# Optimization experiments

Hardware: AMD Instinct MI355X
Metric: run time of the kernel (lower is better)

## Reference

```python
import jax, jax.numpy as jnp
import numpy as np

LN_EPS = 1e-5

def _layer_norm(x, w, b):
    mu = jnp.mean(x, axis=-1, keepdims=True)
    var = jnp.mean(jnp.square(x - mu), axis=-1, keepdims=True)
    return (x - mu) * jax.lax.rsqrt(var + LN_EPS) * w + b

def setup_inputs() -> dict:
    key = jax.random.key(0)
    ks = jax.random.split(key, 8)
    B, NODES, D = 32, 202, 64
    return {
        "embeddings": jax.random.normal(ks[0], (B, NODES, D), dtype=jnp.float32),
        "ln_w": jnp.ones((D,), jnp.float32),
        "ln_b": jnp.zeros((D,), jnp.float32),
        "W1_w": jax.random.normal(ks[1], (D, D), jnp.float32) * 0.05,
        "W1_b": jax.random.normal(ks[2], (D,), jnp.float32) * 0.05,
        "W2_w": jax.random.normal(ks[3], (D, D), jnp.float32) * 0.05,
        "W2_b": jax.random.normal(ks[4], (D,), jnp.float32) * 0.05,
        "a1_w": jax.random.normal(ks[5], (3 * D,), jnp.float32) * 0.05,
        "a1_b": jax.random.normal(ks[6], (1,), jnp.float32) * 0.05,
        "a2_w": jax.random.normal(ks[7], (3 * D,), jnp.float32) * 0.05,
        "a2_b": jax.random.normal(jax.random.fold_in(key, 99), (1,), jnp.float32) * 0.05,
    }

def reference(embeddings, ln_w, ln_b, W1_w, W1_b, W2_w, W2_b, a1_w, a1_b, a2_w, a2_b):
    # embeddings: [B, 2+N, D]; dropout p=0 (eval) -> identity
    emb = _layer_norm(embeddings, ln_w, ln_b)
    uid0 = emb[:, 0, :]          # [B, D]
    iid0 = emb[:, 1, :]          # [B, D]
    iatt = emb[:, 2:, :]         # [B, N, D]
    ua = uid0[:, None, :] * iatt  # [B, N, D]
    # value[b,i,j,:] = LN(ua[b,i] * ua[b,j])  -- the big [B,N,N,D] tensor
    value = _layer_norm(ua[:, :, None, :] * ua[:, None, :, :], ln_w, ln_b)

    def head(Ww, Wb, aw, ab):
        # Linear W applied to expanded query/key/iid collapses to per-row projections;
        # a([wq; wk; wiid]) decomposes additively across the three concat blocks.
        wua = ua @ Ww.T + Wb                  # [B, N, D]  (shared by query rows and key cols)
        wiid = iid0 @ Ww.T + Wb               # [B, D]
        aq, ak, ai = jnp.split(aw, 3)
        sq = wua @ aq                         # [B, N]  query contribution (index i)
        sk = wua @ ak                         # [B, N]  key contribution (index j)
        si = wiid @ ai                        # [B]
        scores = sq[:, :, None] + sk[:, None, :] + si[:, None, None] + ab[0]  # [B,N,N]
        scores = jax.nn.leaky_relu(scores)    # negative_slope=0.01 (torch default)
        alphas = jax.nn.softmax(scores, axis=-1)
        # original sums over dim=-2 (index i), softmax was over j -- kept faithfully
        return jnp.einsum('bij,bijd->bjd', alphas, value)  # [B, N, D]

    att1 = head(W1_w, W1_b, a1_w, a1_b)
    att2 = head(W2_w, W2_b, a2_w, a2_b)
    att_value = (att1 + att2) * 0.5           # [B, N, D]
    ui = (uid0 * iid0)[:, None, :]            # [B, 1, D]
    em_out = jnp.concatenate([ui, att_value], axis=1)  # [B, N+1, D]
    return jax.nn.leaky_relu(em_out)
```

## Files before the change

kernel.cpp:

```cpp
#include <hip/hip_runtime.h>
#include <hip/hip_bf16.h>

#define LN_EPS 1e-5f
#define BB 32
#define NI 200
#define DD 64

typedef __attribute__((ext_vector_type(8))) short bf16x8;
typedef __attribute__((ext_vector_type(4))) short bf16x4;
typedef __attribute__((ext_vector_type(4))) float f32x4;

__device__ __forceinline__ float leaky(float x) { return fmaxf(x, 0.01f * x); }
__device__ __forceinline__ short f2bf(float x) {
  __hip_bfloat16 h = __float2bfloat16(x);
  return *reinterpret_cast<short*>(&h);
}
__device__ __forceinline__ float bf2fs(short s) {
  unsigned u = ((unsigned)(unsigned short)s) << 16;
  return __uint_as_float(u);
}

__device__ __forceinline__ void reduce2(float& a, float& b) {
#pragma unroll
  for (int m = 1; m < 64; m <<= 1) { a += __shfl_xor(a, m, 64); b += __shfl_xor(b, m, 64); }
}
__device__ __forceinline__ void reduce3(float& a, float& b, float& c) {
#pragma unroll
  for (int m = 1; m < 64; m <<= 1) {
    a += __shfl_xor(a, m, 64); b += __shfl_xor(b, m, 64); c += __shfl_xor(c, m, 64);
  }
}
__device__ __forceinline__ void rmax2(float& a, float& b) {
#pragma unroll
  for (int m = 1; m < 64; m <<= 1) {
    a = fmaxf(a, __shfl_xor(a, m, 64));
    b = fmaxf(b, __shfl_xor(b, m, 64));
  }
}

#define WB_STRIDE 88576
#define WB_UA2    26624
#define WB_UAT    53248
#define WB_ST     81920
#define WB_KV     86912
#define WX_RAWD   2834432
#define WX_TD     2940928
#define WX_CR     2941184

__global__ void __launch_bounds__(256)
gat_k1(const float* __restrict__ emb,
       const float* __restrict__ lw,
       const float* __restrict__ lb,
       const float* __restrict__ W1,
       const float* __restrict__ W1b,
       const float* __restrict__ W2,
       const float* __restrict__ W2b,
       const float* __restrict__ a1,
       const float* __restrict__ a2,
       float* __restrict__ ws,
       float* __restrict__ out) {
  __shared__ float sE[18 * 65];
  __shared__ float sV[4 * 64];
  __shared__ float sVi[2 * 64];
  __shared__ float sLN[18 * 2];

  int b = blockIdx.y, it = blockIdx.x, tid = threadIdx.x;
  int wv = tid >> 6, lane = tid & 63;

  char* wsb = (char*)ws + (size_t)b * WB_STRIDE;
  short* wUA  = (short*)wsb;
  short* wUA2 = (short*)(wsb + WB_UA2);
  short* wUAT = (short*)(wsb + WB_UAT);
  float* wRAW = (float*)((char*)ws + WX_RAWD) + (size_t)b * 832;
  float* wTD  = (float*)((char*)ws + WX_TD) + b * 2;
  float* wCR  = (float*)((char*)ws + WX_CR) + b * 6;

  for (int idx = tid; idx < 288; idx += 256) {
    int r = idx >> 4, qd = (idx & 15) << 2;
    int g = (r < 2) ? r : 2 + it * 16 + (r - 2);
    f32x4 v = {0, 0, 0, 0};
    if (g <= 201) v = *(const f32x4*)(emb + ((size_t)b * 202 + g) * 64 + qd);
    float* dst = sE + r * 65 + qd;
    dst[0] = v.x; dst[1] = v.y; dst[2] = v.z; dst[3] = v.w;
  }
  if (wv == 0) {
    float p0 = 0, p1 = 0;
#pragma unroll 8
    for (int d = 0; d < 64; d++) {
      float x = W1[d * 64 + lane];
      p0 = fmaf(x, a1[d], p0); p1 = fmaf(x, a1[64 + d], p1);
    }
    sV[0 * 64 + lane] = p0; sV[1 * 64 + lane] = p1;
  } else if (wv == 1) {
    float p0 = 0, p1 = 0;
#pragma unroll 8
    for (int d = 0; d < 64; d++) {
      float x = W2[d * 64 + lane];
      p0 = fmaf(x, a2[d], p0); p1 = fmaf(x, a2[64 + d], p1);
    }
    sV[2 * 64 + lane] = p0; sV[3 * 64 + lane] = p1;
  } else if (wv == 2 && it == 0) {
    float p = 0;
#pragma unroll 8
    for (int d = 0; d < 64; d++) p = fmaf(W1[d * 64 + lane], a1[128 + d], p);
    sVi[lane] = p;
    float c0 = W1b[lane] * a1[lane];
    float c1 = W1b[lane] * a1[64 + lane];
    float c2 = W1b[lane] * a1[128 + lane];
    reduce3(c0, c1, c2);
    if (lane == 0) { wCR[0] = c0; wCR[1] = c1; wCR[2] = c2; }
  } else if (wv == 3 && it == 0) {
    float p = 0;
#pragma unroll 8
    for (int d = 0; d < 64; d++) p = fmaf(W2[d * 64 + lane], a2[128 + d], p);
    sVi[64 + lane] = p;
    float c3 = W2b[lane] * a2[lane];
    float c4 = W2b[lane] * a2[64 + lane];
    float c5 = W2b[lane] * a2[128 + lane];
    reduce3(c3, c4, c5);
    if (lane == 0) { wCR[3] = c3; wCR[4] = c4; wCR[5] = c5; }
  }
  __syncthreads();

  {
    int o = tid & 7, rr = tid >> 3;
    float s = 0.f, s2 = 0.f;
    if (rr < 18) {
      const float* xr = sE + rr * 65 + o * 8;
#pragma unroll
      for (int k = 0; k < 8; k++) { float x = xr[k]; s += x; s2 = fmaf(x, x, s2); }
    }
#pragma unroll
    for (int m = 1; m < 8; m <<= 1) {
      s += __shfl_xor(s, m, 64); s2 += __shfl_xor(s2, m, 64);
    }
    if (rr < 18 && o == 0) {
      float mu = s * (1.f / 64);
      float var = fmaxf(s2 * (1.f / 64) - mu * mu, 0.f);
      sLN[rr * 2] = mu;
      sLN[rr * 2 + 1] = rsqrtf(var + LN_EPS);
    }
  }
  __syncthreads();

  {
    int d = tid & 63;
    float w = lw[d], bi = lb[d];
    for (int idx = tid; idx < 18 * 64; idx += 256) {
      int r = idx >> 6;
      float mu = sLN[r * 2], rinv = sLN[r * 2 + 1];
      float x = sE[r * 65 + d];
      sE[r * 65 + d] = (x - mu) * rinv * w + bi;
    }
  }
  __syncthreads();

  if (it == 0 && wv == 2) {
    float u0 = sE[lane], iid = sE[65 + lane];
    out[(size_t)(b * 201) * 64 + lane] = leaky(u0 * iid);
    float q0 = iid * sVi[lane], q1 = iid * sVi[64 + lane];
    reduce2(q0, q1);
    if (lane == 0) { wTD[0] = q0; wTD[1] = q1; }
  }
  if (tid < 128) {
    int rem = tid, kh = rem >> 6, ln = rem & 63;
    int lnode = ln & 15, g = it * 16 + lnode;
    int dbase = kh * 32 + (ln >> 4) * 8, lr = 2 + lnode;
    bf16x8 pk, pk2;
    if (g < NI) {
      const float* yr = sE + lr * 65 + dbase;
#pragma unroll
      for (int k = 0; k < 8; k++) {
        float v = sE[dbase + k] * yr[k];
        short h = f2bf(v);
        pk[k] = h;
        float f = bf2fs(h);
        pk2[k] = f2bf(f * f);
      }
    } else {
#pragma unroll
      for (int k = 0; k < 8; k++) { pk[k] = 0; pk2[k] = 0; }
    }
    *(bf16x8*)(wUA + (it * 128 + rem) * 8) = pk;
    *(bf16x8*)(wUA2 + (it * 128 + rem) * 8) = pk2;
  } else {
    int tid2 = tid - 128, d = tid2 & 63;
    int ir = (it & 1) * 2 + (tid2 >> 6), p = it >> 1;
    int i0 = p * 32 + ir * 8, ln0 = i0 - it * 16;
    float ud = sE[d];
    bf16x8 pk;
#pragma unroll
    for (int uu = 0; uu < 8; uu++) {
      int node = i0 + uu;
      pk[uu] = (node < NI) ? f2bf(ud * sE[(2 + ln0 + uu) * 65 + d]) : (short)0;
    }
    int off = ((p * 4 + (d >> 4)) * 64 + ((d & 15) + 16 * ir)) * 8;
    *(bf16x8*)(wUAT + off) = pk;
    if (it == 12) {
      bf16x8 z;
#pragma unroll
      for (int uu = 0; uu < 8; uu++) z[uu] = 0;
      int off2 = ((p * 4 + (d >> 4)) * 64 + ((d & 15) + 16 * (ir + 2))) * 8;
      *(bf16x8*)(wUAT + off2) = z;
    }
  }
  if (tid < 128) {
    int o = tid & 7, rr = tid >> 3;
    int i = it * 16 + rr;
    if (i < NI) {
      float uv0[8], uv1[8], uv2[8], uv3[8];
#pragma unroll
      for (int k = 0; k < 8; k++) {
        float u0k = sE[o * 8 + k];
        uv0[k] = u0k * sV[0 * 64 + o * 8 + k];
        uv1[k] = u0k * sV[1 * 64 + o * 8 + k];
        uv2[k] = u0k * sV[2 * 64 + o * 8 + k];
        uv3[k] = u0k * sV[3 * 64 + o * 8 + k];
      }
      const float* yr = sE + (2 + rr) * 65 + o * 8;
      float p0 = 0, p1 = 0, p2 = 0, p3 = 0;
#pragma unroll
      for (int k = 0; k < 8; k++) {
        float y = yr[k];
        p0 = fmaf(y, uv0[k], p0); p1 = fmaf(y, uv1[k], p1);
        p2 = fmaf(y, uv2[k], p2); p3 = fmaf(y, uv3[k], p3);
      }
#pragma unroll
      for (int m = 1; m < 8; m <<= 1) {
        p0 += __shfl_xor(p0, m, 64); p1 += __shfl_xor(p1, m, 64);
        p2 += __shfl_xor(p2, m, 64); p3 += __shfl_xor(p3, m, 64);
      }
      if (o == 0) {
        wRAW[i * 4 + 0] = p0; wRAW[i * 4 + 1] = p1;
        wRAW[i * 4 + 2] = p2; wRAW[i * 4 + 3] = p3;
      }
    }
  }
}

__global__ void __launch_bounds__(512)
gat_k2(float* __restrict__ ws,
       const float* __restrict__ a1b,
       const float* __restrict__ a2b) {
  __shared__ float skv[2 * 208];
  __shared__ float wmx[16];
  int b = blockIdx.y, bx = blockIdx.x, tid = threadIdx.x;
  int wv = tid >> 6, lane = tid & 63;

  char* wsb = (char*)ws + (size_t)b * WB_STRIDE;
  float* wST = (float*)(wsb + WB_ST);
  float* wKV = (float*)(wsb + WB_KV);
  const float* wRAW = (const float*)((char*)ws + WX_RAWD) + (size_t)b * 832;
  const float* wTD  = (const float*)((char*)ws + WX_TD) + b * 2;
  const float* wCR  = (const float*)((char*)ws + WX_CR) + b * 6;

  float c0 = wCR[0], c1 = wCR[1], c2 = wCR[2];
  float c3 = wCR[3], c4 = wCR[4], c5 = wCR[5];
  float t1 = (wTD[0] + c2) + a1b[0];
  float t2 = (wTD[1] + c5) + a2b[0];

  if (tid < 208) {
    float s1 = 0.f, s2 = 0.f;
    if (tid < NI) {
      s1 = wRAW[tid * 4 + 1] + c1;
      s2 = wRAW[tid * 4 + 3] + c4;
    }
    skv[tid] = s1; skv[208 + tid] = s2;
    if (bx == 0) { wKV[tid] = s1; wKV[208 + tid] = s2; }
  }
  __syncthreads();

  {
    float m1 = (tid < NI) ? skv[tid] : -3e38f;
    float m2 = (tid < NI) ? skv[208 + tid] : -3e38f;
    rmax2(m1, m2);
    if (lane == 0) { wmx[wv * 2] = m1; wmx[wv * 2 + 1] = m2; }
  }
  __syncthreads();

  {
    int o = tid & 3, item = tid >> 2;
    int rl = item >> 1, sh = item & 1;
    if (rl < 52) {
      int r = bx * 52 + rl;
      if (r < 208) {
        float* st = wST + r * 6 + sh * 3;
        if (r < NI) {
          float mx = -3e38f;
#pragma unroll
          for (int k = 0; k < 8; k++) mx = fmaxf(mx, wmx[k * 2 + sh]);
          float base = (wRAW[r * 4 + (sh ? 2 : 0)] + (sh ? c3 : c0)) + (sh ? t2 : t1);
          float rm = leaky(base + mx);
          const float* skh = skv + sh * 208;
          float den = 0.f;
          int j0 = o * 50;
#pragma unroll 5
          for (int j = j0; j < j0 + 50; j++) {
            float s = base + skh[j];
            den += __expf(fmaxf(s, 0.01f * s) - rm);
          }
          den += __shfl_xor(den, 1, 64);
          den += __shfl_xor(den, 2, 64);
          if (o == 0) { st[0] = base; st[1] = rm; st[2] = 1.0f / den; }
        } else if (o == 0) {
          st[0] = 0.f; st[1] = 0.f; st[2] = 0.f;
        }
      }
    }
  }
}

#define L_G1    7168
#define L_STAGE 14336
#define L_UA    14336
#define L_UA2   40960
#define L_UAT   67584
#define L_ST    96256
#define L_KV    101248
#define L_PART  102912
#define L_TOTAL 103936

__global__ void __launch_bounds__(512, 1)
gat_k3(const float* __restrict__ ws,
       const float* __restrict__ lw,
       const float* __restrict__ lb,
       float* __restrict__ out) {
  __shared__ __align__(16) char smem[L_TOTAL];
  short* sUA  = (short*)(smem + L_UA);
  short* sUA2 = (short*)(smem + L_UA2);
  short* sUAT = (short*)(smem + L_UAT);
  float* sST  = (float*)(smem + L_ST);
  float* sKV  = (float*)(smem + L_KV);
  float* sPart = (float*)(smem + L_PART);

  int b = blockIdx.y, bx = blockIdx.x, tid = threadIdx.x;
  int wv = tid >> 6, lane = tid & 63, q = lane >> 4, col = lane & 15;

  {
    const f32x4* src = (const f32x4*)((const char*)ws + (size_t)b * WB_STRIDE);
    f32x4* dst = (f32x4*)(smem + L_STAGE);
    for (int idx = tid; idx < WB_STRIDE / 16; idx += 512) dst[idx] = src[idx];
  }
  short* sG0 = (short*)smem;
  short* sG1 = (short*)(smem + L_G1);
  if (tid < 128) ((int*)sG0)[1664 + tid] = 0;
  else if (tid < 256) ((int*)sG1)[1664 + (tid - 128)] = 0;
  __syncthreads();

  int half = wv >> 2, wq = wv & 3;
  int jt = bx * 2 + half;
  bool act = (jt < 13);
  short* sGh = half ? sG1 : sG0;
  float* sPh = sPart + half * 128;

  if (act) {
    bf16x8 bf0 = *(bf16x8*)(sUA + ((jt * 2 + 0) * 64 + lane) * 8);
    bf16x8 bf1 = *(bf16x8*)(sUA + ((jt * 2 + 1) * 64 + lane) * 8);
    bf16x8 b2f0 = *(bf16x8*)(sUA2 + ((jt * 2 + 0) * 64 + lane) * 8);
    bf16x8 b2f1 = *(bf16x8*)(sUA2 + ((jt * 2 + 1) * 64 + lane) * 8);
    int jglob = jt * 16 + col;
    float skj1 = sKV[jglob], skj2 = sKV[208 + jglob];
    float mpart = 0.f, spart = 0.f;
    for (int it = wq; it < 13; it += 4) {
      bf16x8 af0 = *(bf16x8*)(sUA + ((it * 2 + 0) * 64 + lane) * 8);
      bf16x8 af1 = *(bf16x8*)(sUA + ((it * 2 + 1) * 64 + lane) * 8);
      bf16x8 a2f0 = *(bf16x8*)(sUA2 + ((it * 2 + 0) * 64 + lane) * 8);
      bf16x8 a2f1 = *(bf16x8*)(sUA2 + ((it * 2 + 1) * 64 + lane) * 8);
      f32x4 s = {0, 0, 0, 0}, t = {0, 0, 0, 0};
      s = __builtin_amdgcn_mfma_f32_16x16x32_bf16(af0, bf0, s, 0, 0, 0);
      s = __builtin_amdgcn_mfma_f32_16x16x32_bf16(af1, bf1, s, 0, 0, 0);
      t = __builtin_amdgcn_mfma_f32_16x16x32_bf16(a2f0, b2f0, t, 0, 0, 0);
      t = __builtin_amdgcn_mfma_f32_16x16x32_bf16(a2f1, b2f1, t, 0, 0, 0);
      bf16x4 gp;
#pragma unroll
      for (int r = 0; r < 4; r++) {
        int i = it * 16 + q * 4 + r;
        const float* st = sST + i * 6;
        float mu = s[r] * (1.f / 64);
        float var = fmaxf(t[r] * (1.f / 64) - mu * mu, 0.f);
        float inv = rsqrtf(var + LN_EPS);
        float sc1 = st[0] + skj1;
        float e1 = __expf(fmaxf(sc1, 0.01f * sc1) - st[1]) * st[2];
        float sc2 = st[3] + skj2;
        float e2 = __expf(fmaxf(sc2, 0.01f * sc2) - st[4]) * st[5];
        float c = 0.5f * (e1 + e2);
        float g = c * inv;
        mpart = fmaf(g, mu, mpart);
        spart += c;
        gp[r] = f2bf(g);
      }
      int kl = (it & 1) * 16 + q * 4;
      int off = ((it >> 1) * 64 + (col + 16 * (kl >> 3))) * 8 + (kl & 7);
      *(bf16x4*)(sGh + off) = gp;
    }
    mpart += __shfl_xor(mpart, 16, 64); mpart += __shfl_xor(mpart, 32, 64);
    spart += __shfl_xor(spart, 16, 64); spart += __shfl_xor(spart, 32, 64);
    if (lane < 16) {
      sPh[(wq * 2 + 0) * 16 + lane] = mpart;
      sPh[(wq * 2 + 1) * 16 + lane] = spart;
    }
  }
  __syncthreads();

  if (act) {
    f32x4 acc = {0, 0, 0, 0};
#pragma unroll
    for (int kt = 0; kt < 7; kt++) {
      bf16x8 ga = *(bf16x8*)(sGh + (kt * 64 + lane) * 8);
      bf16x8 ub = *(bf16x8*)(sUAT + ((kt * 4 + wq) * 64 + lane) * 8);
      acc = __builtin_amdgcn_mfma_f32_16x16x32_bf16(ga, ub, acc, 0, 0, 0);
    }
    int d = wq * 16 + col;
    float w = lw[d], bia = lb[d];
#pragma unroll
    for (int r = 0; r < 4; r++) {
      int jl = q * 4 + r, jg = jt * 16 + jl;
      if (jg < NI) {
        float m = sPh[0 * 16 + jl] + sPh[2 * 16 + jl] +
                  sPh[4 * 16 + jl] + sPh[6 * 16 + jl];
        float S = sPh[1 * 16 + jl] + sPh[3 * 16 + jl] +
                  sPh[5 * 16 + jl] + sPh[7 * 16 + jl];
        int cn = jt * 128 + (d >> 5) * 64 + ((d >> 3) & 3) * 16 + (jg & 15);
        float uajd = bf2fs(sUA[cn * 8 + (d & 7)]);
        float att = w * (uajd * acc[r] - m) + bia * S;
        out[(size_t)(b * 201 + 1 + jg) * 64 + d] = leaky(att);
      }
    }
  }
}

extern "C" void kernel_launch(void* const* d_in, const int* in_sizes, int n_in,
                              void* d_out, int out_size, void* d_ws, size_t ws_size,
                              hipStream_t stream) {
  const float* emb = (const float*)d_in[0];
  const float* lw  = (const float*)d_in[1];
  const float* lb  = (const float*)d_in[2];
  const float* W1  = (const float*)d_in[3];
  const float* W1b = (const float*)d_in[4];
  const float* W2  = (const float*)d_in[5];
  const float* W2b = (const float*)d_in[6];
  const float* a1  = (const float*)d_in[7];
  const float* a1b = (const float*)d_in[8];
  const float* a2  = (const float*)d_in[9];
  const float* a2b = (const float*)d_in[10];
  float* ws = (float*)d_ws;
  float* out = (float*)d_out;

  gat_k1<<<dim3(13, BB), dim3(256), 0, stream>>>(emb, lw, lb, W1, W1b, W2, W2b,
                                                 a1, a2, ws, out);
  gat_k2<<<dim3(4, BB), dim3(512), 0, stream>>>(ws, a1b, a2b);
  gat_k3<<<dim3(7, BB), dim3(512), 0, stream>>>(ws, lw, lb, out);
}
```

Measured before the change: 93.90 us.

## Fuse three kernels into one cooperative kernel with grid-wide syncs

Merges the three separate kernels into a single cooperative launch on a 7x32 grid of 512-thread blocks. Each block runs two former stage-1 tiles, one per half-block. Grid-wide syncs replace the kernel boundaries between the projection, softmax-statistics and attention stages. The softmax-denominator stage now spreads 30 rows per block across 7 blocks instead of 52 rows across 4. This removes two kernel launch gaps, at the cost of grid barrier overhead and a co-residency requirement of 224 blocks with about 104KB of LDS each.

```diff
diff --git a/kernel.cpp b/kernel.cpp
--- a/kernel.cpp
+++ b/kernel.cpp
@@ -1,5 +1,8 @@
 #include <hip/hip_runtime.h>
 #include <hip/hip_bf16.h>
+#include <hip/hip_cooperative_groups.h>
+
+namespace cg = cooperative_groups;
 
 #define LN_EPS 1e-5f
 #define BB 32
@@ -42,46 +45,77 @@
 #define WB_UA2    26624
 #define WB_UAT    53248
 #define WB_ST     81920
-#define WB_KV     86912
+#define WB_STAGE  86912
 #define WX_RAWD   2834432
 #define WX_TD     2940928
 #define WX_CR     2941184
 
-__global__ void __launch_bounds__(256)
-gat_k1(const float* __restrict__ emb,
-       const float* __restrict__ lw,
-       const float* __restrict__ lb,
-       const float* __restrict__ W1,
-       const float* __restrict__ W1b,
-       const float* __restrict__ W2,
-       const float* __restrict__ W2b,
-       const float* __restrict__ a1,
-       const float* __restrict__ a2,
-       float* __restrict__ ws,
-       float* __restrict__ out) {
-  __shared__ float sE[18 * 65];
-  __shared__ float sV[4 * 64];
-  __shared__ float sVi[2 * 64];
-  __shared__ float sLN[18 * 2];
-
-  int b = blockIdx.y, it = blockIdx.x, tid = threadIdx.x;
-  int wv = tid >> 6, lane = tid & 63;
+#define L_G1    7168
+#define L_SE0   0
+#define L_SE1   4680
+#define L_SV    9360
+#define L_SVI   10384
+#define L_SLN   10896
+#define L_STAGE 14336
+#define L_UA    14336
+#define L_UA2   40960
+#define L_UAT   67584
+#define L_ST    96256
+#define L_KV    101248
+#define L_PART  102912
+#define L_TOTAL 103936
+
+__global__ void __launch_bounds__(512, 1)
+gat_coop(const float* __restrict__ emb,
+         const float* __restrict__ lw,
+         const float* __restrict__ lb,
+         const float* __restrict__ W1,
+         const float* __restrict__ W1b,
+         const float* __restrict__ W2,
+         const float* __restrict__ W2b,
+         const float* __restrict__ a1,
+         const float* __restrict__ a1b,
+         const float* __restrict__ a2,
+         const float* __restrict__ a2b,
+         float* __restrict__ ws,
+         float* __restrict__ out) {
+  __shared__ __align__(16) char smem[L_TOTAL];
+  float* sV   = (float*)(smem + L_SV);
+  float* sVi  = (float*)(smem + L_SVI);
+  short* sUA  = (short*)(smem + L_UA);
+  short* sUA2 = (short*)(smem + L_UA2);
+  short* sUAT = (short*)(smem + L_UAT);
+  float* sST  = (float*)(smem + L_ST);
+  float* sKV  = (float*)(smem + L_KV);
+  float* sPart = (float*)(smem + L_PART);
+
+  int b = blockIdx.y, bx = blockIdx.x, tid = threadIdx.x;
+  int wv = tid >> 6, lane = tid & 63, q = lane >> 4, col = lane & 15;
+  int th = tid >> 8, t2 = tid & 255;
 
   char* wsb = (char*)ws + (size_t)b * WB_STRIDE;
   short* wUA  = (short*)wsb;
   short* wUA2 = (short*)(wsb + WB_UA2);
   short* wUAT = (short*)(wsb + WB_UAT);
+  float* wST  = (float*)(wsb + WB_ST);
   float* wRAW = (float*)((char*)ws + WX_RAWD) + (size_t)b * 832;
   float* wTD  = (float*)((char*)ws + WX_TD) + b * 2;
   float* wCR  = (float*)((char*)ws + WX_CR) + b * 6;
 
-  for (int idx = tid; idx < 288; idx += 256) {
-    int r = idx >> 4, qd = (idx & 15) << 2;
-    int g = (r < 2) ? r : 2 + it * 16 + (r - 2);
-    f32x4 v = {0, 0, 0, 0};
-    if (g <= 201) v = *(const f32x4*)(emb + ((size_t)b * 202 + g) * 64 + qd);
-    float* dst = sE + r * 65 + qd;
-    dst[0] = v.x; dst[1] = v.y; dst[2] = v.z; dst[3] = v.w;
+  int it = bx * 2 + th;
+  bool act1 = (it < 13);
+  float* sE = (float*)(smem + (th ? L_SE1 : L_SE0));
+  float* sLN = (float*)(smem + L_SLN) + th * 36;
+
+  if (act1) {
+    for (int idx = t2; idx < 288; idx += 256) {
+      int r = idx >> 4, qd = (idx & 15) << 2;
+      int g = (r < 2) ? r : 2 + it * 16 + (r - 2);
+      f32x4 v = {0, 0, 0, 0};
+      if (g <= 201) v = *(const f32x4*)(emb + ((size_t)b * 202 + g) * 64 + qd);
+      float* dst = sE + r * 65 + qd;
+      dst[0] = v.x; dst[1] = v.y; dst[2] = v.z; dst[3] = v.w;
+    }
   }
   if (wv == 0) {
     float p0 = 0, p1 = 0;
@@ -99,7 +133,7 @@
       p0 = fmaf(x, a2[d], p0); p1 = fmaf(x, a2[64 + d], p1);
     }
     sV[2 * 64 + lane] = p0; sV[3 * 64 + lane] = p1;
-  } else if (wv == 2 && it == 0) {
+  } else if (wv == 2 && bx == 0) {
     float p = 0;
 #pragma unroll 8
     for (int d = 0; d < 64; d++) p = fmaf(W1[d * 64 + lane], a1[128 + d], p);
@@ -109,7 +143,7 @@
     float c2 = W1b[lane] * a1[128 + lane];
     reduce3(c0, c1, c2);
     if (lane == 0) { wCR[0] = c0; wCR[1] = c1; wCR[2] = c2; }
-  } else if (wv == 3 && it == 0) {
+  } else if (wv == 3 && bx == 0) {
     float p = 0;
 #pragma unroll 8
     for (int d = 0; d < 64; d++) p = fmaf(W2[d * 64 + lane], a2[128 + d], p);
@@ -123,9 +157,9 @@
   __syncthreads();
 
   {
-    int o = tid & 7, rr = tid >> 3;
+    int o = t2 & 7, rr = t2 >> 3;
     float s = 0.f, s2 = 0.f;
-    if (rr < 18) {
+    if (act1 && rr < 18) {
       const float* xr = sE + rr * 65 + o * 8;
 #pragma unroll
       for (int k = 0; k < 8; k++) { float x = xr[k]; s += x; s2 = fmaf(x, x, s2); }
@@ -134,7 +168,7 @@
     for (int m = 1; m < 8; m <<= 1) {
       s += __shfl_xor(s, m, 64); s2 += __shfl_xor(s2, m, 64);
     }
-    if (rr < 18 && o == 0) {
+    if (act1 && rr < 18 && o == 0) {
       float mu = s * (1.f / 64);
       float var = fmaxf(s2 * (1.f / 64) - mu * mu, 0.f);
       sLN[rr * 2] = mu;
@@ -143,10 +177,10 @@
   }
   __syncthreads();
 
-  {
-    int d = tid & 63;
+  if (act1) {
+    int d = t2 & 63;
     float w = lw[d], bi = lb[d];
-    for (int idx = tid; idx < 18 * 64; idx += 256) {
+    for (int idx = t2; idx < 18 * 64; idx += 256) {
       int r = idx >> 6;
       float mu = sLN[r * 2], rinv = sLN[r * 2 + 1];
       float x = sE[r * 65 + d];
@@ -155,191 +189,156 @@
   }
   __syncthreads();
 
-  if (it == 0 && wv == 2) {
-    float u0 = sE[lane], iid = sE[65 + lane];
+  if (bx == 0 && wv == 2) {
+    const float* sE0 = (const float*)(smem + L_SE0);
+    float u0 = sE0[lane], iid = sE0[65 + lane];
     out[(size_t)(b * 201) * 64 + lane] = leaky(u0 * iid);
     float q0 = iid * sVi[lane], q1 = iid * sVi[64 + lane];
     reduce2(q0, q1);
     if (lane == 0) { wTD[0] = q0; wTD[1] = q1; }
   }
-  if (tid < 128) {
-    int rem = tid, kh = rem >> 6, ln = rem & 63;
-    int lnode = ln & 15, g = it * 16 + lnode;
-    int dbase = kh * 32 + (ln >> 4) * 8, lr = 2 + lnode;
-    bf16x8 pk, pk2;
-    if (g < NI) {
-      const float* yr = sE + lr * 65 + dbase;
-#pragma unroll
-      for (int k = 0; k < 8; k++) {
-        float v = sE[dbase + k] * yr[k];
-        short h = f2bf(v);
-        pk[k] = h;
-        float f = bf2fs(h);
-        pk2[k] = f2bf(f * f);
-      }
+  if (act1) {
+    if (t2 < 128) {
+      int rem = t2, kh = rem >> 6, ln = rem & 63;
+      int lnode = ln & 15, g = it * 16 + lnode;
+      int dbase = kh * 32 + (ln >> 4) * 8, lr = 2 + lnode;
+      bf16x8 pk, pk2;
+      if (g < NI) {
+        const float* yr = sE + lr * 65 + dbase;
+#pragma unroll
+        for (int k = 0; k < 8; k++) {
+          float v = sE[dbase + k] * yr[k];
+          short h = f2bf(v);
+          pk[k] = h;
+          float f = bf2fs(h);
+          pk2[k] = f2bf(f * f);
+        }
+      } else {
+#pragma unroll
+        for (int k = 0; k < 8; k++) { pk[k] = 0; pk2[k] = 0; }
+      }
+      *(bf16x8*)(wUA + (it * 128 + rem) * 8) = pk;
+      *(bf16x8*)(wUA2 + (it * 128 + rem) * 8) = pk2;
     } else {
-#pragma unroll
-      for (int k = 0; k < 8; k++) { pk[k] = 0; pk2[k] = 0; }
-    }
-    *(bf16x8*)(wUA + (it * 128 + rem) * 8) = pk;
-    *(bf16x8*)(wUA2 + (it * 128 + rem) * 8) = pk2;
-  } else {
-    int tid2 = tid - 128, d = tid2 & 63;
-    int ir = (it & 1) * 2 + (tid2 >> 6), p = it >> 1;
-    int i0 = p * 32 + ir * 8, ln0 = i0 - it * 16;
-    float ud = sE[d];
-    bf16x8 pk;
-#pragma unroll
-    for (int uu = 0; uu < 8; uu++) {
-      int node = i0 + uu;
-      pk[uu] = (node < NI) ? f2bf(ud * sE[(2 + ln0 + uu) * 65 + d]) : (short)0;
-    }
-    int off = ((p * 4 + (d >> 4)) * 64 + ((d & 15) + 16 * ir)) * 8;
-    *(bf16x8*)(wUAT + off) = pk;
-    if (it == 12) {
-      bf16x8 z;
-#pragma unroll
-      for (int uu = 0; uu < 8; uu++) z[uu] = 0;
-      int off2 = ((p * 4 + (d >> 4)) * 64 + ((d & 15) + 16 * (ir + 2))) * 8;
-      *(bf16x8*)(wUAT + off2) = z;
-    }
-  }
-  if (tid < 128) {
-    int o = tid & 7, rr = tid >> 3;
-    int i = it * 16 + rr;
-    if (i < NI) {
-      float uv0[8], uv1[8], uv2[8], uv3[8];
-#pragma unroll
-      for (int k = 0; k < 8; k++) {
-        float u0k = sE[o * 8 + k];
-        uv0[k] = u0k * sV[0 * 64 + o * 8 + k];
-        uv1[k] = u0k * sV[1 * 64 + o * 8 + k];
-        uv2[k] = u0k * sV[2 * 64 + o * 8 + k];
-        uv3[k] = u0k * sV[3 * 64 + o * 8 + k];
-      }
-      const float* yr = sE + (2 + rr) * 65 + o * 8;
-      float p0 = 0, p1 = 0, p2 = 0, p3 = 0;
-#pragma unroll
-      for (int k = 0; k < 8; k++) {
-        float y = yr[k];
-        p0 = fmaf(y, uv0[k], p0); p1 = fmaf(y, uv1[k], p1);
-        p2 = fmaf(y, uv2[k], p2); p3 = fmaf(y, uv3[k], p3);
-      }
-#pragma unroll
-      for (int m = 1; m < 8; m <<= 1) {
-        p0 += __shfl_xor(p0, m, 64); p1 += __shfl_xor(p1, m, 64);
-        p2 += __shfl_xor(p2, m, 64); p3 += __shfl_xor(p3, m, 64);
-      }
-      if (o == 0) {
-        wRAW[i * 4 + 0] = p0; wRAW[i * 4 + 1] = p1;
-        wRAW[i * 4 + 2] = p2; wRAW[i * 4 + 3] = p3;
-      }
-    }
-  }
-}
-
-__global__ void __launch_bounds__(512)
-gat_k2(float* __restrict__ ws,
-       const float* __restrict__ a1b,
-       const float* __restrict__ a2b) {
-  __shared__ float skv[2 * 208];
-  __shared__ float wmx[16];
-  int b = blockIdx.y, bx = blockIdx.x, tid = threadIdx.x;
-  int wv = tid >> 6, lane = tid & 63;
-
-  char* wsb = (char*)ws + (size_t)b * WB_STRIDE;
-  float* wST = (float*)(wsb + WB_ST);
-  float* wKV = (float*)(wsb + WB_KV);
-  const float* wRAW = (const float*)((char*)ws + WX_RAWD) + (size_t)b * 832;
-  const float* wTD  = (const float*)((char*)ws + WX_TD) + b * 2;
-  const float* wCR  = (const float*)((char*)ws + WX_CR) + b * 6;
-
-  float c0 = wCR[0], c1 = wCR[1], c2 = wCR[2];
-  float c3 = wCR[3], c4 = wCR[4], c5 = wCR[5];
-  float t1 = (wTD[0] + c2) + a1b[0];
-  float t2 = (wTD[1] + c5) + a2b[0];
-
-  if (tid < 208) {
-    float s1 = 0.f, s2 = 0.f;
-    if (tid < NI) {
-      s1 = wRAW[tid * 4 + 1] + c1;
-      s2 = wRAW[tid * 4 + 3] + c4;
-    }
-    skv[tid] = s1; skv[208 + tid] = s2;
-    if (bx == 0) { wKV[tid] = s1; wKV[208 + tid] = s2; }
-  }
-  __syncthreads();
+      int tid2 = t2 - 128, d = tid2 & 63;
+      int ir = (it & 1) * 2 + (tid2 >> 6), p = it >> 1;
+      int i0 = p * 32 + ir * 8, ln0 = i0 - it * 16;
+      float ud = sE[d];
+      bf16x8 pk;
+#pragma unroll
+      for (int uu = 0; uu < 8; uu++) {
+        int node = i0 + uu;
+        pk[uu] = (node < NI) ? f2bf(ud * sE[(2 + ln0 + uu) * 65 + d]) : (short)0;
+      }
+      int off = ((p * 4 + (d >> 4)) * 64 + ((d & 15) + 16 * ir)) * 8;
+      *(bf16x8*)(wUAT + off) = pk;
+      if (it == 12) {
+        bf16x8 z;
+#pragma unroll
+        for (int uu = 0; uu < 8; uu++) z[uu] = 0;
+        int off2 = ((p * 4 + (d >> 4)) * 64 + ((d & 15) + 16 * (ir + 2))) * 8;
+        *(bf16x8*)(wUAT + off2) = z;
+      }
+    }
+    if (t2 < 128) {
+      int o = t2 & 7, rr = t2 >> 3;
+      int i = it * 16 + rr;
+      if (i < NI) {
+        float uv0[8], uv1[8], uv2[8], uv3[8];
+#pragma unroll
+        for (int k = 0; k < 8; k++) {
+          float u0k = sE[o * 8 + k];
+          uv0[k] = u0k * sV[0 * 64 + o * 8 + k];
+          uv1[k] = u0k * sV[1 * 64 + o * 8 + k];
+          uv2[k] = u0k * sV[2 * 64 + o * 8 + k];
+          uv3[k] = u0k * sV[3 * 64 + o * 8 + k];
+        }
+        const float* yr = sE + (2 + rr) * 65 + o * 8;
+        float p0 = 0, p1 = 0, p2 = 0, p3 = 0;
+#pragma unroll
+        for (int k = 0; k < 8; k++) {
+          float y = yr[k];
+          p0 = fmaf(y, uv0[k], p0); p1 = fmaf(y, uv1[k], p1);
+          p2 = fmaf(y, uv2[k], p2); p3 = fmaf(y, uv3[k], p3);
+        }
+#pragma unroll
+        for (int m = 1; m < 8; m <<= 1) {
+          p0 += __shfl_xor(p0, m, 64); p1 += __shfl_xor(p1, m, 64);
+          p2 += __shfl_xor(p2, m, 64); p3 += __shfl_xor(p3, m, 64);
+        }
+        if (o == 0) {
+          wRAW[i * 4 + 0] = p0; wRAW[i * 4 + 1] = p1;
+          wRAW[i * 4 + 2] = p2; wRAW[i * 4 + 3] = p3;
+        }
+      }
+    }
+  }
+
+  cg::this_grid().sync();
 
   {
-    float m1 = (tid < NI) ? skv[tid] : -3e38f;
-    float m2 = (tid < NI) ? skv[208 + tid] : -3e38f;
-    rmax2(m1, m2);
-    if (lane == 0) { wmx[wv * 2] = m1; wmx[wv * 2 + 1] = m2; }
-  }
-  __syncthreads();
+    float c0 = wCR[0], c1 = wCR[1], c2 = wCR[2];
+    float c3 = wCR[3], c4 = wCR[4], c5 = wCR[5];
+    float t1 = (wTD[0] + c2) + a1b[0];
+    float t2h = (wTD[1] + c5) + a2b[0];
+
+    if (tid < 208) {
+      float s1 = 0.f, s2 = 0.f;
+      if (tid < NI) {
+        s1 = wRAW[tid * 4 + 1] + c1;
+        s2 = wRAW[tid * 4 + 3] + c4;
+      }
+      sKV[tid] = s1; sKV[208 + tid] = s2;
+    }
+    __syncthreads();
+
+    float* wmx = sPart;
+    {
+      float m1 = (tid < NI) ? sKV[tid] : -3e38f;
+      float m2 = (tid < NI) ? sKV[208 + tid] : -3e38f;
+      rmax2(m1, m2);
+      if (lane == 0) { wmx[wv * 2] = m1; wmx[wv * 2 + 1] = m2; }
+    }
+    __syncthreads();
+
+    {
+      int o = tid & 3, item = tid >> 2;
+      int rl = item >> 1, sh = item & 1;
+      if (rl < 30) {
+        int r = bx * 30 + rl;
+        if (r < 208) {
+          float* st = wST + r * 6 + sh * 3;
+          if (r < NI) {
+            float mx = -3e38f;
+#pragma unroll
+            for (int k = 0; k < 8; k++) mx = fmaxf(mx, wmx[k * 2 + sh]);
+            float base = (wRAW[r * 4 + (sh ? 2 : 0)] + (sh ? c3 : c0)) + (sh ? t2h : t1);
+            float rm = leaky(base + mx);
+            const float* skh = sKV + sh * 208;
+            float den = 0.f;
+            int j0 = o * 50;
+#pragma unroll 5
+            for (int j = j0; j < j0 + 50; j++) {
+              float s = base + skh[j];
+              den += __expf(fmaxf(s, 0.01f * s) - rm);
+            }
+            den += __shfl_xor(den, 1, 64);
+            den += __shfl_xor(den, 2, 64);
+            if (o == 0) { st[0] = base; st[1] = rm; st[2] = 1.0f / den; }
+          } else if (o == 0) {
+            st[0] = 0.f; st[1] = 0.f; st[2] = 0.f;
+          }
+        }
+      }
+    }
+  }
+
+  cg::this_grid().sync();
 
   {
-    int o = tid & 3, item = tid >> 2;
-    int rl = item >> 1, sh = item & 1;
-    if (rl < 52) {
-      int r = bx * 52 + rl;
-      if (r < 208) {
-        float* st = wST + r * 6 + sh * 3;
-        if (r < NI) {
-          float mx = -3e38f;
-#pragma unroll
-          for (int k = 0; k < 8; k++) mx = fmaxf(mx, wmx[k * 2 + sh]);
-          float base = (wRAW[r * 4 + (sh ? 2 : 0)] + (sh ? c3 : c0)) + (sh ? t2 : t1);
-          float rm = leaky(base + mx);
-          const float* skh = skv + sh * 208;
-          float den = 0.f;
-          int j0 = o * 50;
-#pragma unroll 5
-          for (int j = j0; j < j0 + 50; j++) {
-            float s = base + skh[j];
-            den += __expf(fmaxf(s, 0.01f * s) - rm);
-          }
-          den += __shfl_xor(den, 1, 64);
-          den += __shfl_xor(den, 2, 64);
-          if (o == 0) { st[0] = base; st[1] = rm; st[2] = 1.0f / den; }
-        } else if (o == 0) {
-          st[0] = 0.f; st[1] = 0.f; st[2] = 0.f;
-        }
-      }
-    }
-  }
-}
-
-#define L_G1    7168
-#define L_STAGE 14336
-#define L_UA    14336
-#define L_UA2   40960
-#define L_UAT   67584
-#define L_ST    96256
-#define L_KV    101248
-#define L_PART  102912
-#define L_TOTAL 103936
-
-__global__ void __launch_bounds__(512, 1)
-gat_k3(const float* __restrict__ ws,
-       const float* __restrict__ lw,
-       const float* __restrict__ lb,
-       float* __restrict__ out) {
-  __shared__ __align__(16) char smem[L_TOTAL];
-  short* sUA  = (short*)(smem + L_UA);
-  short* sUA2 = (short*)(smem + L_UA2);
-  short* sUAT = (short*)(smem + L_UAT);
-  float* sST  = (float*)(smem + L_ST);
-  float* sKV  = (float*)(smem + L_KV);
-  float* sPart = (float*)(smem + L_PART);
-
-  int b = blockIdx.y, bx = blockIdx.x, tid = threadIdx.x;
-  int wv = tid >> 6, lane = tid & 63, q = lane >> 4, col = lane & 15;
-
-  {
-    const f32x4* src = (const f32x4*)((const char*)ws + (size_t)b * WB_STRIDE);
+    const f32x4* src = (const f32x4*)wsb;
     f32x4* dst = (f32x4*)(smem + L_STAGE);
-    for (int idx = tid; idx < WB_STRIDE / 16; idx += 512) dst[idx] = src[idx];
+    for (int idx = tid; idx < WB_STAGE / 16; idx += 512) dst[idx] = src[idx];
   }
   short* sG0 = (short*)smem;
   short* sG1 = (short*)(smem + L_G1);
@@ -361,11 +360,11 @@
     int jglob = jt * 16 + col;
     float skj1 = sKV[jglob], skj2 = sKV[208 + jglob];
     float mpart = 0.f, spart = 0.f;
-    for (int it = wq; it < 13; it += 4) {
-      bf16x8 af0 = *(bf16x8*)(sUA + ((it * 2 + 0) * 64 + lane) * 8);
-      bf16x8 af1 = *(bf16x8*)(sUA + ((it * 2 + 1) * 64 + lane) * 8);
-      bf16x8 a2f0 = *(bf16x8*)(sUA2 + ((it * 2 + 0) * 64 + lane) * 8);
-      bf16x8 a2f1 = *(bf16x8*)(sUA2 + ((it * 2 + 1) * 64 + lane) * 8);
+    for (int it2 = wq; it2 < 13; it2 += 4) {
+      bf16x8 af0 = *(bf16x8*)(sUA + ((it2 * 2 + 0) * 64 + lane) * 8);
+      bf16x8 af1 = *(bf16x8*)(sUA + ((it2 * 2 + 1) * 64 + lane) * 8);
+      bf16x8 a2f0 = *(bf16x8*)(sUA2 + ((it2 * 2 + 0) * 64 + lane) * 8);
+      bf16x8 a2f1 = *(bf16x8*)(sUA2 + ((it2 * 2 + 1) * 64 + lane) * 8);
       f32x4 s = {0, 0, 0, 0}, t = {0, 0, 0, 0};
       s = __builtin_amdgcn_mfma_f32_16x16x32_bf16(af0, bf0, s, 0, 0, 0);
       s = __builtin_amdgcn_mfma_f32_16x16x32_bf16(af1, bf1, s, 0, 0, 0);
@@ -374,7 +373,7 @@
       bf16x4 gp;
 #pragma unroll
       for (int r = 0; r < 4; r++) {
-        int i = it * 16 + q * 4 + r;
+        int i = it2 * 16 + q * 4 + r;
         const float* st = sST + i * 6;
         float mu = s[r] * (1.f / 64);
         float var = fmaxf(t[r] * (1.f / 64) - mu * mu, 0.f);
@@ -389,8 +388,8 @@
         spart += c;
         gp[r] = f2bf(g);
       }
-      int kl = (it & 1) * 16 + q * 4;
-      int off = ((it >> 1) * 64 + (col + 16 * (kl >> 3))) * 8 + (kl & 7);
+      int kl = (it2 & 1) * 16 + q * 4;
+      int off = ((it2 >> 1) * 64 + (col + 16 * (kl >> 3))) * 8 + (kl & 7);
       *(bf16x4*)(sGh + off) = gp;
     }
     mpart += __shfl_xor(mpart, 16, 64); mpart += __shfl_xor(mpart, 32, 64);
@@ -446,8 +445,9 @@
   float* ws = (float*)d_ws;
   float* out = (float*)d_out;
 
-  gat_k1<<<dim3(13, BB), dim3(256), 0, stream>>>(emb, lw, lb, W1, W1b, W2, W2b,
-                                                 a1, a2, ws, out);
-  gat_k2<<<dim3(4, BB), dim3(512), 0, stream>>>(ws, a1b, a2b);
-  gat_k3<<<dim3(7, BB), dim3(512), 0, stream>>>(ws, lw, lb, out);
-}
+  void* args[] = {(void*)&emb, (void*)&lw, (void*)&lb, (void*)&W1, (void*)&W1b,
+                  (void*)&W2, (void*)&W2b, (void*)&a1, (void*)&a1b, (void*)&a2,
+                  (void*)&a2b, (void*)&ws, (void*)&out};
+  hipLaunchCooperativeKernel((const void*)gat_coop, dim3(7, BB), dim3(512),
+                             args, 0, stream);
+}
```

After: 162.0 us. 72.5% more time.
